# Kernel tuning notes

Measured on AMD Instinct MI355X. Metric: run time of the kernel, lower is better.

The kernel has to match this reference:

```python
import jax, jax.numpy as jnp
import numpy as np

B, T, C, H = 2, 2048, 1024, 16
Dh = C // H  # 64
EPS = 1e-5


def layer_norm(x, g, b):
    mu = jnp.mean(x, axis=-1, keepdims=True)
    var = jnp.mean(jnp.square(x - mu), axis=-1, keepdims=True)
    return (x - mu) * jax.lax.rsqrt(var + EPS) * g + b


def setup_inputs() -> dict:
    key = jax.random.key(0)
    ks = jax.random.split(key, 12)
    s = 0.02
    return {
        "x": jax.random.normal(ks[0], (B, T, C), dtype=jnp.float32),
        # per-head projections, stacked: (H, C, Dh), no bias (bias=False in source)
        "Wq": jax.random.normal(ks[1], (H, C, Dh), dtype=jnp.float32) * s,
        "Wk": jax.random.normal(ks[2], (H, C, Dh), dtype=jnp.float32) * s,
        "Wv": jax.random.normal(ks[3], (H, C, Dh), dtype=jnp.float32) * s,
        "Wo": jax.random.normal(ks[4], (H * Dh, C), dtype=jnp.float32) * s,
        "bo": jnp.zeros((C,), dtype=jnp.float32),
        "W1": jax.random.normal(ks[5], (C, 4 * C), dtype=jnp.float32) * s,
        "b1": jnp.zeros((4 * C,), dtype=jnp.float32),
        "W2": jax.random.normal(ks[6], (4 * C, C), dtype=jnp.float32) * s,
        "b2": jnp.zeros((C,), dtype=jnp.float32),
        "g1": jnp.ones((C,), dtype=jnp.float32),
        "be1": jnp.zeros((C,), dtype=jnp.float32),
        "g2": jnp.ones((C,), dtype=jnp.float32),
        "be2": jnp.zeros((C,), dtype=jnp.float32),
    }


def reference(x, Wq, Wk, Wv, Wo, bo, W1, b1, W2, b2, g1, be1, g2, be2):
    # --- self-attention sublayer ---
    h = layer_norm(x, g1, be1)                       # (B,T,C)
    q = jnp.einsum("btc,hcd->bhtd", h, Wq)
    k = jnp.einsum("btc,hcd->bhtd", h, Wk)
    v = jnp.einsum("btc,hcd->bhtd", h, Wv)
    # NOTE: source scales by C**-0.5 (head INPUT dim), not head_size**-0.5
    scores = jnp.einsum("bhqd,bhkd->bhqk", q, k) * (C ** -0.5)
    # encoder=True default => mask is all ones => no masking applied
    w = jax.nn.softmax(scores, axis=-1)              # (B,H,T,T)
    o = jnp.einsum("bhqk,bhkd->bhqd", w, v)          # (B,H,T,Dh)
    o = o.transpose(0, 2, 1, 3).reshape(B, T, H * Dh)  # concat heads
    attn = o @ Wo + bo                               # output projection
    x = x + attn
    # --- feed-forward sublayer ---
    h2 = layer_norm(x, g2, be2)
    ff = jax.nn.relu(h2 @ W1 + b1) @ W2 + b2
    return x + ff
```

## Files before the change

### kernel.cpp

```cpp
#include <hip/hip_runtime.h>
#include <hip/hip_bf16.h>

#define BT   4096
#define CD   1024
#define TD   2048
#define NH   16
#define DH   64
#define BB   2

typedef __attribute__((ext_vector_type(8))) short bf16x8;
typedef __attribute__((ext_vector_type(4))) short bf16x4;
typedef __attribute__((ext_vector_type(4))) float f32x4;
typedef __attribute__((ext_vector_type(2))) unsigned int u32x2;
typedef __attribute__((ext_vector_type(4))) unsigned int u32x4;

__device__ inline short f2bf(float f) {
    union { float fv; unsigned u; } x; x.fv = f;
    unsigned r = x.u + 0x7fffu + ((x.u >> 16) & 1u);
    return (short)(r >> 16);
}
__device__ inline float bf2f(short s) {
    union { unsigned u; float f; } x; x.u = ((unsigned)(unsigned short)s) << 16;
    return x.f;
}
__device__ inline unsigned pk2bf(float a, float b) {
    union { __hip_bfloat162 h; unsigned u; } cv;
    cv.h = __float22bfloat162_rn(float2{a, b});
    return cv.u;
}

#if __has_builtin(__builtin_amdgcn_exp2f)
#define EXP2(x) __builtin_amdgcn_exp2f(x)
#else
#define EXP2(x) exp2f(x)
#endif

__device__ inline void gload_lds16(const short* g, short* lds) {
    __builtin_amdgcn_global_load_lds(
        (const __attribute__((address_space(1))) void*)g,
        (__attribute__((address_space(3))) void*)lds, 16, 0, 0);
}

__launch_bounds__(256)
__global__ void ln_kernel(const float* __restrict__ x,
                          const float* __restrict__ g,
                          const float* __restrict__ be,
                          short* __restrict__ out) {
    __shared__ float red[2][4];
    const int row = blockIdx.x;
    const int c4 = threadIdx.x * 4;
    const float* xr = x + (size_t)row * CD;
    float4 v = *(const float4*)&xr[c4];
    float s  = (v.x + v.y) + (v.z + v.w);
    float ss = (v.x * v.x + v.y * v.y) + (v.z * v.z + v.w * v.w);
    #pragma unroll
    for (int off = 32; off > 0; off >>= 1) {
        s  += __shfl_down(s,  off, 64);
        ss += __shfl_down(ss, off, 64);
    }
    int wid = threadIdx.x >> 6, lane = threadIdx.x & 63;
    if (lane == 0) { red[0][wid] = s; red[1][wid] = ss; }
    __syncthreads();
    float sum   = red[0][0] + red[0][1] + red[0][2] + red[0][3];
    float sumsq = red[1][0] + red[1][1] + red[1][2] + red[1][3];
    float mu   = sum * (1.f / CD);
    float var  = sumsq * (1.f / CD) - mu * mu;
    float rstd = rsqrtf(var + 1e-5f);
    float4 gv = *(const float4*)&g[c4];
    float4 bv = *(const float4*)&be[c4];
    bf16x4 o;
    o[0] = f2bf((v.x - mu) * rstd * gv.x + bv.x);
    o[1] = f2bf((v.y - mu) * rstd * gv.y + bv.y);
    o[2] = f2bf((v.z - mu) * rstd * gv.z + bv.z);
    o[3] = f2bf((v.w - mu) * rstd * gv.w + bv.w);
    *(bf16x4*)&out[(size_t)row * CD + c4] = o;
}

__launch_bounds__(256)
__global__ void prep_weights(const float* __restrict__ Wq, const float* __restrict__ Wk,
                             const float* __restrict__ Wv, const float* __restrict__ Wo,
                             const float* __restrict__ W1, const float* __restrict__ W2,
                             short* __restrict__ wqt, short* __restrict__ wot,
                             short* __restrict__ w1t, short* __restrict__ w2t) {
    __shared__ float tt[64][65];
    const int id = blockIdx.x;
    const float* in; short* out; int R, Cc, r0, c0;
    if (id < 768) {
        int which = id >> 8, rem = id & 255, hh = rem >> 4, ry = rem & 15;
        in  = (which == 0 ? Wq : which == 1 ? Wk : Wv) + (size_t)hh * CD * DH;
        out = wqt + (size_t)which * CD * CD + (size_t)hh * DH * CD;
        R = CD; Cc = DH; r0 = ry * 64; c0 = 0;
    } else if (id < 1024) {
        int t = id - 768;  in = Wo; out = wot; R = CD;     Cc = CD;     r0 = (t >> 4) * 64; c0 = (t & 15) * 64;
    } else if (id < 2048) {
        int t = id - 1024; in = W1; out = w1t; R = CD;     Cc = 4 * CD; r0 = (t >> 6) * 64; c0 = (t & 63) * 64;
    } else {
        int t = id - 2048; in = W2; out = w2t; R = 4 * CD; Cc = CD;     r0 = (t >> 4) * 64; c0 = (t & 15) * 64;
    }
    const int tid = threadIdx.x;
    #pragma unroll
    for (int i = 0; i < 4; ++i) {
        int f = i * 256 + tid;
        int r = f >> 4, cc = (f & 15) * 4;
        float4 vv = *(const float4*)&in[(size_t)(r0 + r) * Cc + c0 + cc];
        tt[r][cc]     = vv.x;
        tt[r][cc + 1] = vv.y;
        tt[r][cc + 2] = vv.z;
        tt[r][cc + 3] = vv.w;
    }
    __syncthreads();
    #pragma unroll
    for (int i = 0; i < 16; ++i) {
        int e = i * 256 + tid;
        out[(size_t)(c0 + (e >> 6)) * R + r0 + (e & 63)] = f2bf(tt[e & 63][e >> 6]);
    }
}

__launch_bounds__(256)
__global__ void vtrans(const short* __restrict__ vin, short* __restrict__ vout) {
    __shared__ short t[64 * 65];
    const int tid = threadIdx.x;
    const int bh = blockIdx.y;
    const int t0 = blockIdx.x * 64;
    const int b = bh >> 4, h = bh & 15;
    const short* src = vin + (size_t)b * TD * CD + (size_t)h * DH;
    short* dst = vout + (size_t)bh * DH * TD;
    #pragma unroll
    for (int i = 0; i < 16; ++i) {
        int e = i * 256 + tid;
        t[(e >> 6) * 65 + (e & 63)] = src[(size_t)(t0 + (e >> 6)) * CD + (e & 63)];
    }
    __syncthreads();
    #pragma unroll
    for (int i = 0; i < 16; ++i) {
        int e = i * 256 + tid;
        int d = e >> 6, tt = e & 63;
        dst[(size_t)d * TD + t0 + tt] = t[tt * 65 + d];
    }
}

template <int MODE, int TN, int GR>
__launch_bounds__(GR * 256)
__global__ void gemm_mfma(const short* __restrict__ A,
                          const short* __restrict__ Bt,
                          const float* __restrict__ bias,
                          const float* __restrict__ resid,
                          float* __restrict__ outf,
                          short* __restrict__ outb,
                          int N, int K) {
    constexpr int NBUF = (GR == 2) ? 4 : 3;
    __shared__ __align__(16) short smem[GR * NBUF * (128 + TN) * 32];
    const int tid = threadIdx.x;
    const int kgrp = (GR == 2) ? (tid >> 8) : 0;
    const int tid256 = tid & 255;
    const int w4 = tid256 >> 6, lane = tid & 63;
    const int quad = lane >> 4, l16 = lane & 15;
    const int wr = w4 >> 1, wc = w4 & 1;
    const int li = blockIdx.y * gridDim.x + blockIdx.x;
    const int m0 = ((li & 7) * 4 + ((li >> 3) & 3)) * 128;
    const int n0 = (li >> 5) * TN;
    const int NT = TN / 32;
    const int kbase = kgrp * (K / GR);

    short* grpBase = smem + (size_t)kgrp * NBUF * (128 + TN) * 32;
#define AS(bi) (grpBase + (bi) * (128 + TN) * 32)
#define BS(bi) (AS(bi) + 128 * 32)

    f32x4 acc[4][NT] = {};

    auto STAGE = [&](int kt, int bi) {
        const int k0 = kbase + kt * 32;
        short* as = AS(bi);
        short* bs = BS(bi);
        #pragma unroll
        for (int i = 0; i < 2; ++i) {
            int s = i * 256 + tid256;
            int row = s >> 2, kc = (s & 3) ^ ((row >> 1) & 3);
            gload_lds16(A + (size_t)(m0 + row) * K + k0 + kc * 8,
                        &as[(i * 256 + w4 * 64) * 8]);
        }
        #pragma unroll
        for (int i = 0; i < TN / 64; ++i) {
            int s = i * 256 + tid256;
            int row = s >> 2, kc = (s & 3) ^ ((row >> 1) & 3);
            gload_lds16(Bt + (size_t)(n0 + row) * K + k0 + kc * 8,
                        &bs[(i * 256 + w4 * 64) * 8]);
        }
    };

    auto COMPUTE = [&](int bi) {
        const int xo = (quad ^ ((l16 >> 1) & 3)) * 8;
        const short* as = AS(bi);
        const short* bs = BS(bi);
        bf16x8 a[4], b[NT];
        #pragma unroll
        for (int mt = 0; mt < 4; ++mt)
            a[mt] = *(const bf16x8*)&as[(wr * 64 + mt * 16 + l16) * 32 + xo];
        #pragma unroll
        for (int nt = 0; nt < NT; ++nt)
            b[nt] = *(const bf16x8*)&bs[(wc * (TN / 2) + nt * 16 + l16) * 32 + xo];
        #pragma unroll
        for (int mt = 0; mt < 4; ++mt)
            #pragma unroll
            for (int nt = 0; nt < NT; ++nt)
                acc[mt][nt] = __builtin_amdgcn_mfma_f32_16x16x32_bf16(a[mt], b[nt], acc[mt][nt], 0, 0, 0);
    };

    const int nk = (K / GR) >> 5;
    if (GR == 2) {
        STAGE(0, 0);
        STAGE(1, 1);
        STAGE(2, 2);
        for (int t = 0; t < nk - 2; ++t) {
            asm volatile("s_waitcnt vmcnt(8)" ::: "memory");
            __builtin_amdgcn_s_barrier();
            asm volatile("" ::: "memory");
            if (t + 3 < nk) STAGE(t + 3, (t + 3) & 3);
            COMPUTE(t & 3);
        }
        asm volatile("s_waitcnt vmcnt(4)" ::: "memory");
        __builtin_amdgcn_s_barrier();
        asm volatile("" ::: "memory");
        COMPUTE((nk - 2) & 3);
        asm volatile("s_waitcnt vmcnt(0)" ::: "memory");
        __builtin_amdgcn_s_barrier();
        asm volatile("" ::: "memory");
        COMPUTE((nk - 1) & 3);
    } else {
        STAGE(0, 0);
        STAGE(1, 1);
        int bi = 0;
        for (int t = 0; t < nk - 1; ++t) {
            if (TN == 256) asm volatile("s_waitcnt vmcnt(6)" ::: "memory");
            else           asm volatile("s_waitcnt vmcnt(4)" ::: "memory");
            __builtin_amdgcn_s_barrier();
            asm volatile("" ::: "memory");
            int bn = bi + 2 >= 3 ? bi - 1 : bi + 2;
            if (t + 2 < nk) STAGE(t + 2, bn);
            COMPUTE(bi);
            bi = bi + 1 >= 3 ? 0 : bi + 1;
        }
        asm volatile("s_waitcnt vmcnt(0)" ::: "memory");
        __builtin_amdgcn_s_barrier();
        asm volatile("" ::: "memory");
        COMPUTE(bi);
    }

    if (GR == 2) {
        float* red = (float*)smem;
        __syncthreads();
        if (kgrp == 1) {
            #pragma unroll
            for (int mt = 0; mt < 4; ++mt)
                #pragma unroll
                for (int nt = 0; nt < NT; ++nt)
                    *(f32x4*)&red[((mt * NT + nt) * 256 + w4 * 64 + lane) * 4] = acc[mt][nt];
        }
        __syncthreads();
        if (kgrp == 1) return;
        #pragma unroll
        for (int mt = 0; mt < 4; ++mt)
            #pragma unroll
            for (int nt = 0; nt < NT; ++nt) {
                f32x4 p = *(const f32x4*)&red[((mt * NT + nt) * 256 + w4 * 64 + lane) * 4];
                acc[mt][nt] += p;
            }
    }

    const float qsc = (MODE == 5 && n0 < CD) ? 0.03125f * 1.44269504f : 1.0f;
    short* ob5 = (MODE == 5) ? outb + (size_t)(n0 >> 10) * BT * CD : nullptr;

    #pragma unroll
    for (int mt = 0; mt < 4; ++mt)
        #pragma unroll
        for (int nt = 0; nt < NT; ++nt)
            #pragma unroll
            for (int reg = 0; reg < 4; ++reg) {
                int row = m0 + wr * 64 + mt * 16 + quad * 4 + reg;
                int col = n0 + wc * (TN / 2) + nt * 16 + l16;
                float v = acc[mt][nt][reg];
                if (MODE == 1) { v += bias[col] + resid[(size_t)row * N + col];
                                 outf[(size_t)row * N + col] = v; }
                if (MODE == 2) { v = fmaxf(v + bias[col], 0.f);
                                 outb[(size_t)row * N + col] = f2bf(v); }
                if (MODE == 5) { ob5[(size_t)row * CD + (col & 1023)] = f2bf(v * qsc); }
            }
#undef AS
#undef BS
}

#define BQ   128
#define BK   32

__launch_bounds__(256, 5)
__global__ void attn_mfma(const short* __restrict__ q,
                          const short* __restrict__ k,
                          const short* __restrict__ vt,
                          short* __restrict__ opart,
                          float* __restrict__ lpart) {
    __shared__ short Ks[4][BK * DH];
    __shared__ short Vt[4][DH * BK];

    const int tid  = threadIdx.x;
    const int w = tid >> 6, lane = tid & 63;
    const int quad = lane >> 4, l16 = lane & 15;
    const int h = blockIdx.y;
    const int b = blockIdx.z >> 1, split = blockIdx.z & 1;
    const int q0 = blockIdx.x * BQ;
    const size_t base  = (size_t)b * TD * CD + (size_t)h * DH;
    const size_t vbase = (size_t)(b * NH + h) * DH * TD;

    bf16x8 qf[2][2];
    #pragma unroll
    for (int rt = 0; rt < 2; ++rt) {
        const short* qp = q + base + (size_t)(q0 + w * 32 + rt * 16 + l16) * CD;
        qf[rt][0] = *(const bf16x8*)&qp[quad * 8];
        qf[rt][1] = *(const bf16x8*)&qp[32 + quad * 8];
    }

    const bf16x8 ones = {(short)0x3F80, (short)0x3F80, (short)0x3F80, (short)0x3F80,
                         (short)0x3F80, (short)0x3F80, (short)0x3F80, (short)0x3F80};
    f32x4 O_l[2] = {};
    f32x4 O[2][4] = {};

    const int kbeg = split * (TD / 2);
    const int NTI = (TD / 2) / BK;

    const int ks  = tid >> 3;
    const int kc  = (tid & 7) ^ (ks & 7);
    const int kkey = (((ks & 15) >> 2) << 3) + (ks & 3) + ((ks >> 4) << 2);
    const short* kgp = k + base + (size_t)kkey * CD + kc * 8;
    const int vd = tid >> 2;
    const int vc = (tid & 3) ^ ((vd >> 1) & 3);
    const short* vgp = vt + vbase + (size_t)vd * TD + vc * 8;

#define STAGE_T(kt, bi) do {                                              \
        const size_t ko_ = (size_t)(kbeg + (kt) * BK);                    \
        gload_lds16(kgp + ko_ * CD, &Ks[bi][w * 512]);                    \
        gload_lds16(vgp + ko_,      &Vt[bi][w * 512]);                    \
    } while (0)

#define COMPUTE_T(bi) do {                                                \
        __builtin_amdgcn_s_setprio(1);                                    \
        const int kswz = l16 & 7;                                         \
        bf16x8 kbe0 = *(const bf16x8*)&Ks[bi][l16 * 64 + ((quad) ^ kswz) * 8];        \
        bf16x8 kbe1 = *(const bf16x8*)&Ks[bi][l16 * 64 + ((4 + quad) ^ kswz) * 8];    \
        bf16x8 kbo0 = *(const bf16x8*)&Ks[bi][(16 + l16) * 64 + ((quad) ^ kswz) * 8]; \
        bf16x8 kbo1 = *(const bf16x8*)&Ks[bi][(16 + l16) * 64 + ((4 + quad) ^ kswz) * 8]; \
        bf16x8 pa8[2];                                                    \
        _Pragma("unroll")                                                 \
        for (int rt = 0; rt < 2; ++rt) {                                  \
            f32x4 ae = (f32x4){0.f, 0.f, 0.f, 0.f};                       \
            f32x4 ao = (f32x4){0.f, 0.f, 0.f, 0.f};                       \
            ae = __builtin_amdgcn_mfma_f32_16x16x32_bf16(kbe0, qf[rt][0], ae, 0, 0, 0); \
            ae = __builtin_amdgcn_mfma_f32_16x16x32_bf16(kbe1, qf[rt][1], ae, 0, 0, 0); \
            ao = __builtin_amdgcn_mfma_f32_16x16x32_bf16(kbo0, qf[rt][0], ao, 0, 0, 0); \
            ao = __builtin_amdgcn_mfma_f32_16x16x32_bf16(kbo1, qf[rt][1], ao, 0, 0, 0); \
            float pe0 = EXP2(ae[0]), pe1 = EXP2(ae[1]);                   \
            float pe2 = EXP2(ae[2]), pe3 = EXP2(ae[3]);                   \
            float po0 = EXP2(ao[0]), po1 = EXP2(ao[1]);                   \
            float po2 = EXP2(ao[2]), po3 = EXP2(ao[3]);                   \
            union { u32x4 u; bf16x8 s; } cv_;                             \
            cv_.u = (u32x4){pk2bf(pe0, pe1), pk2bf(pe2, pe3),             \
                            pk2bf(po0, po1), pk2bf(po2, po3)};            \
            pa8[rt] = cv_.s;                                              \
        }                                                                 \
        const int vswz = (l16 >> 1) & 3;                                  \
        _Pragma("unroll")                                                 \
        for (int dt = 0; dt < 4; ++dt) {                                  \
            bf16x8 vb = *(const bf16x8*)&Vt[bi][(dt * 16 + l16) * 32 + ((quad) ^ vswz) * 8]; \
            O[0][dt] = __builtin_amdgcn_mfma_f32_16x16x32_bf16(pa8[0], vb, O[0][dt], 0, 0, 0); \
            O[1][dt] = __builtin_amdgcn_mfma_f32_16x16x32_bf16(pa8[1], vb, O[1][dt], 0, 0, 0); \
        }                                                                 \
        O_l[0] = __builtin_amdgcn_mfma_f32_16x16x32_bf16(pa8[0], ones, O_l[0], 0, 0, 0); \
        O_l[1] = __builtin_amdgcn_mfma_f32_16x16x32_bf16(pa8[1], ones, O_l[1], 0, 0, 0); \
        __builtin_amdgcn_s_setprio(0);                                    \
    } while (0)

    STAGE_T(0, 0);
    STAGE_T(1, 1);
    STAGE_T(2, 2);
    for (int t = 0; t < NTI - 2; ++t) {
        asm volatile("s_waitcnt vmcnt(4)" ::: "memory");
        __builtin_amdgcn_s_barrier();
        asm volatile("" ::: "memory");
        if (t + 3 < NTI) STAGE_T(t + 3, (t + 3) & 3);
        COMPUTE_T(t & 3);
    }
    asm volatile("s_waitcnt vmcnt(2)" ::: "memory");
    __builtin_amdgcn_s_barrier();
    asm volatile("" ::: "memory");
    COMPUTE_T((NTI - 2) & 3);
    asm volatile("s_waitcnt vmcnt(0)" ::: "memory");
    __builtin_amdgcn_s_barrier();
    asm volatile("" ::: "memory");
    COMPUTE_T((NTI - 1) & 3);
#undef STAGE_T
#undef COMPUTE_T

    short* osp = opart + (size_t)split * BT * CD;
    float* lsp = lpart + (size_t)split * BB * NH * TD + (size_t)(b * NH + h) * TD;
    #pragma unroll
    for (int rt = 0; rt < 2; ++rt) {
        if (l16 == 0)
            *(f32x4*)&lsp[q0 + w * 32 + rt * 16 + quad * 4] = O_l[rt];
        #pragma unroll
        for (int reg = 0; reg < 4; ++reg) {
            int row = q0 + w * 32 + rt * 16 + quad * 4 + reg;
            short* op = osp + base + (size_t)row * CD;
            #pragma unroll
            for (int dt = 0; dt < 4; ++dt)
                op[dt * 16 + l16] = f2bf(O[rt][dt][reg]);
        }
    }
}

__launch_bounds__(256)
__global__ void attn_combine(const short* __restrict__ opart,
                             const float* __restrict__ lpart,
                             short* __restrict__ ob) {
    const size_t idx = ((size_t)blockIdx.x * 256 + threadIdx.x) * 8;
    const int row = (int)(idx >> 10);
    const int col = (int)(idx & 1023);
    const int b = row >> 11, qq = row & (TD - 1), hh = col >> 6;
    const size_t lbase = (size_t)(b * NH + hh) * TD + qq;
    const float l0 = lpart[lbase];
    const float l1 = lpart[(size_t)BB * NH * TD + lbase];
    const float inv = 1.f / (l0 + l1);
    bf16x8 a = *(const bf16x8*)&opart[idx];
    bf16x8 c = *(const bf16x8*)&opart[(size_t)BT * CD + idx];
    bf16x8 r;
    #pragma unroll
    for (int j = 0; j < 8; ++j)
        r[j] = f2bf((bf2f(a[j]) + bf2f(c[j])) * inv);
    *(bf16x8*)&ob[idx] = r;
}

extern "C" void kernel_launch(void* const* d_in, const int* in_sizes, int n_in,
                              void* d_out, int out_size, void* d_ws, size_t ws_size,
                              hipStream_t stream) {
    const float* x   = (const float*)d_in[0];
    const float* Wq  = (const float*)d_in[1];
    const float* Wk  = (const float*)d_in[2];
    const float* Wv  = (const float*)d_in[3];
    const float* Wo  = (const float*)d_in[4];
    const float* bo  = (const float*)d_in[5];
    const float* W1  = (const float*)d_in[6];
    const float* b1  = (const float*)d_in[7];
    const float* W2  = (const float*)d_in[8];
    const float* b2  = (const float*)d_in[9];
    const float* g1  = (const float*)d_in[10];
    const float* be1 = (const float*)d_in[11];
    const float* g2  = (const float*)d_in[12];
    const float* be2 = (const float*)d_in[13];
    float* out = (float*)d_out;

    const size_t SZ = (size_t)BT * CD;
    float* ws  = (float*)d_ws;
    short* qbf = (short*)ws;
    short* kbf = qbf + SZ;
    short* vbf = qbf + 2 * SZ;
    float* lpart = ws + SZ + SZ / 2;
    short* opart = (short*)(ws + 2 * SZ);
    float* x1  = ws + 2 * SZ;
    short* h   = (short*)(ws + 3 * SZ);
    short* ob  = (short*)(ws + 3 * SZ + SZ / 2);
    short* wqt = (short*)(ws + 4 * SZ);
    short* wot = wqt + 3 * CD * CD;
    short* w1t = (short*)(ws + 4 * SZ + SZ / 2);
    short* w2t = (short*)(ws + 5 * SZ);
    short* vtg = (short*)(ws + 5 * SZ + SZ / 2);
    short* ff1 = (short*)ws;

    ln_kernel<<<BT, 256, 0, stream>>>(x, g1, be1, h);

    prep_weights<<<3072, 256, 0, stream>>>(Wq, Wk, Wv, Wo, W1, W2, wqt, wot, w1t, w2t);

    gemm_mfma<5, 128, 1><<<dim3(24, 32), 256, 0, stream>>>(h, wqt, nullptr, nullptr, nullptr, qbf, 3 * CD, CD);

    vtrans<<<dim3(TD / 64, 2 * NH), 256, 0, stream>>>(vbf, vtg);

    attn_mfma<<<dim3(TD / BQ, NH, BB * 2), 256, 0, stream>>>(qbf, kbf, vtg, opart, lpart);

    attn_combine<<<dim3((int)(SZ / (256 * 8))), 256, 0, stream>>>(opart, lpart, ob);

    gemm_mfma<1, 128, 2><<<dim3(8, 32), 512, 0, stream>>>(ob, wot, bo, x, x1, nullptr, CD, CD);

    ln_kernel<<<BT, 256, 0, stream>>>(x1, g2, be2, h);

    gemm_mfma<2, 256, 1><<<dim3(16, 32), 256, 0, stream>>>(h, w1t, b1, nullptr, nullptr, ff1, 4 * CD, CD);

    gemm_mfma<1, 128, 2><<<dim3(8, 32), 512, 0, stream>>>(ff1, w2t, b2, x1, out, nullptr, CD, 4 * CD);
}
```

Baseline: 322.5 us.

## Split W2 GEMM K across four wave groups and shrink attention pipeline depth

Adds a GR=4 intra-block split-K variant of the MFMA GEMM. It uses 1024 threads, double buffering, and a staged shared-memory reduction across the four K groups, and applies it to the FFN down-projection (K=4096). The attention kernel drops from four to three K/V LDS buffers with a rotating prefetch of depth two, which cuts LDS use per block and may allow more resident blocks. In exchange, the split-K path adds barriers and reduction traffic, and the shallower prefetch in attention can expose more memory latency.

```diff
diff --git a/kernel.cpp b/kernel.cpp
--- a/kernel.cpp
+++ b/kernel.cpp
@@ -148,10 +148,10 @@
                           float* __restrict__ outf,
                           short* __restrict__ outb,
                           int N, int K) {
-    constexpr int NBUF = (GR == 2) ? 4 : 3;
+    constexpr int NBUF = (GR == 2) ? 4 : ((GR == 4) ? 2 : 3);
     __shared__ __align__(16) short smem[GR * NBUF * (128 + TN) * 32];
     const int tid = threadIdx.x;
-    const int kgrp = (GR == 2) ? (tid >> 8) : 0;
+    const int kgrp = (GR > 1) ? (tid >> 8) : 0;
     const int tid256 = tid & 255;
     const int w4 = tid256 >> 6, lane = tid & 63;
     const int quad = lane >> 4, l16 = lane & 15;
@@ -207,7 +207,23 @@
     };
 
     const int nk = (K / GR) >> 5;
-    if (GR == 2) {
+    if (GR == 4) {
+        STAGE(0, 0);
+        STAGE(1, 1);
+        for (int t = 0; t < nk - 1; ++t) {
+            asm volatile("s_waitcnt vmcnt(4)" ::: "memory");
+            __builtin_amdgcn_s_barrier();
+            asm volatile("" ::: "memory");
+            COMPUTE(t & 1);
+            __builtin_amdgcn_s_barrier();
+            asm volatile("" ::: "memory");
+            if (t + 2 < nk) STAGE(t + 2, t & 1);
+        }
+        asm volatile("s_waitcnt vmcnt(0)" ::: "memory");
+        __builtin_amdgcn_s_barrier();
+        asm volatile("" ::: "memory");
+        COMPUTE((nk - 1) & 1);
+    } else if (GR == 2) {
         STAGE(0, 0);
         STAGE(1, 1);
         STAGE(2, 2);
@@ -246,7 +262,30 @@
         COMPUTE(bi);
     }
 
-    if (GR == 2) {
+    if (GR == 4) {
+        float* red = (float*)smem;
+        #pragma unroll
+        for (int mt = 0; mt < 4; ++mt) {
+            __syncthreads();
+            if (kgrp != 0) {
+                #pragma unroll
+                for (int nt = 0; nt < NT; ++nt)
+                    *(f32x4*)&red[(size_t)(kgrp - 1) * 4096 + (nt * 256 + w4 * 64 + lane) * 4] = acc[mt][nt];
+            }
+            __syncthreads();
+            if (kgrp == 0) {
+                #pragma unroll
+                for (int nt = 0; nt < NT; ++nt) {
+                    int off = (nt * 256 + w4 * 64 + lane) * 4;
+                    f32x4 p1 = *(const f32x4*)&red[off];
+                    f32x4 p2 = *(const f32x4*)&red[4096 + off];
+                    f32x4 p3 = *(const f32x4*)&red[8192 + off];
+                    acc[mt][nt] += (p1 + p2) + p3;
+                }
+            }
+        }
+        if (kgrp != 0) return;
+    } else if (GR == 2) {
         float* red = (float*)smem;
         __syncthreads();
         if (kgrp == 1) {
@@ -298,8 +337,8 @@
                           const short* __restrict__ vt,
                           short* __restrict__ opart,
                           float* __restrict__ lpart) {
-    __shared__ short Ks[4][BK * DH];
-    __shared__ short Vt[4][DH * BK];
+    __shared__ short Ks[3][BK * DH];
+    __shared__ short Vt[3][DH * BK];
 
     const int tid  = threadIdx.x;
     const int w = tid >> 6, lane = tid & 63;
@@ -379,22 +418,20 @@
 
     STAGE_T(0, 0);
     STAGE_T(1, 1);
-    STAGE_T(2, 2);
-    for (int t = 0; t < NTI - 2; ++t) {
-        asm volatile("s_waitcnt vmcnt(4)" ::: "memory");
+    int bi = 0;
+    for (int t = 0; t < NTI - 1; ++t) {
+        asm volatile("s_waitcnt vmcnt(2)" ::: "memory");
         __builtin_amdgcn_s_barrier();
         asm volatile("" ::: "memory");
-        if (t + 3 < NTI) STAGE_T(t + 3, (t + 3) & 3);
-        COMPUTE_T(t & 3);
-    }
-    asm volatile("s_waitcnt vmcnt(2)" ::: "memory");
-    __builtin_amdgcn_s_barrier();
-    asm volatile("" ::: "memory");
-    COMPUTE_T((NTI - 2) & 3);
+        int bn = bi + 2 >= 3 ? bi - 1 : bi + 2;
+        if (t + 2 < NTI) STAGE_T(t + 2, bn);
+        COMPUTE_T(bi);
+        bi = bi + 1 >= 3 ? 0 : bi + 1;
+    }
     asm volatile("s_waitcnt vmcnt(0)" ::: "memory");
     __builtin_amdgcn_s_barrier();
     asm volatile("" ::: "memory");
-    COMPUTE_T((NTI - 1) & 3);
+    COMPUTE_T(bi);
 #undef STAGE_T
 #undef COMPUTE_T
 
@@ -490,5 +527,5 @@
 
     gemm_mfma<2, 256, 1><<<dim3(16, 32), 256, 0, stream>>>(h, w1t, b1, nullptr, nullptr, ff1, 4 * CD, CD);
 
-    gemm_mfma<1, 128, 2><<<dim3(8, 32), 512, 0, stream>>>(ff1, w2t, b2, x1, out, nullptr, CD, 4 * CD);
-}
+    gemm_mfma<1, 128, 4><<<dim3(8, 32), 1024, 0, stream>>>(ff1, w2t, b2, x1, out, nullptr, CD, 4 * CD);
+}
```

Result: no change. 328.1 us (+1.7%).

## Add 256x256-tile GEMM for FFN up-projection and triple-buffer attention pipeline

Applied to the files above, without the earlier changes.

Adds a new 512-thread GEMM kernel with 256x256 output tiles, 3-stage LDS buffering and a swizzled block-to-tile mapping, and uses it for the W1 up-projection with bias and ReLU. Larger tiles raise arithmetic intensity and cut redundant global loads of A and B. The attention kernel also moves from a 4-deep to a 3-deep K/V ring buffer with prefetch distance 2, which lowers LDS use and may raise occupancy but hides less latency. The new GEMM launches only 256 blocks at one block per CU, so occupancy is low.

```diff
diff --git a/kernel.cpp b/kernel.cpp
--- a/kernel.cpp
+++ b/kernel.cpp
@@ -289,6 +289,97 @@
 #undef BS
 }
 
+__launch_bounds__(512, 1)
+__global__ void gemm_256(const short* __restrict__ A,
+                         const short* __restrict__ Bt,
+                         const float* __restrict__ bias,
+                         short* __restrict__ outb,
+                         int N, int K) {
+    __shared__ __align__(16) short smem[3 * 512 * 32];
+    const int tid = threadIdx.x;
+    const int w = tid >> 6, lane = tid & 63;
+    const int quad = lane >> 4, l16 = lane & 15;
+    const int wr = w >> 2, wc = w & 3;
+    const int li = blockIdx.x;
+    const int m0 = ((li & 7) * 2 + ((li >> 3) & 1)) * 256;
+    const int n0 = (li >> 4) * 256;
+
+#define AS6(bi) (smem + (bi) * 512 * 32)
+#define BS6(bi) (AS6(bi) + 256 * 32)
+
+    f32x4 acc[8][4] = {};
+
+    auto STAGE = [&](int kt, int bi) {
+        const int k0 = kt * 32;
+        short* as = AS6(bi);
+        short* bs = BS6(bi);
+        #pragma unroll
+        for (int i = 0; i < 2; ++i) {
+            int s = i * 512 + tid;
+            int row = s >> 2, kc = (s & 3) ^ ((row >> 1) & 3);
+            gload_lds16(A + (size_t)(m0 + row) * K + k0 + kc * 8,
+                        &as[(i * 512 + w * 64) * 8]);
+        }
+        #pragma unroll
+        for (int i = 0; i < 2; ++i) {
+            int s = i * 512 + tid;
+            int row = s >> 2, kc = (s & 3) ^ ((row >> 1) & 3);
+            gload_lds16(Bt + (size_t)(n0 + row) * K + k0 + kc * 8,
+                        &bs[(i * 512 + w * 64) * 8]);
+        }
+    };
+
+    auto COMPUTE = [&](int bi) {
+        const int xo = (quad ^ ((l16 >> 1) & 3)) * 8;
+        const short* as = AS6(bi);
+        const short* bs = BS6(bi);
+        bf16x8 a[8], b[4];
+        #pragma unroll
+        for (int mt = 0; mt < 8; ++mt)
+            a[mt] = *(const bf16x8*)&as[(wr * 128 + mt * 16 + l16) * 32 + xo];
+        #pragma unroll
+        for (int nt = 0; nt < 4; ++nt)
+            b[nt] = *(const bf16x8*)&bs[(wc * 64 + nt * 16 + l16) * 32 + xo];
+        #pragma unroll
+        for (int mt = 0; mt < 8; ++mt)
+            #pragma unroll
+            for (int nt = 0; nt < 4; ++nt)
+                acc[mt][nt] = __builtin_amdgcn_mfma_f32_16x16x32_bf16(a[mt], b[nt], acc[mt][nt], 0, 0, 0);
+    };
+
+    const int nk = K >> 5;
+    STAGE(0, 0);
+    STAGE(1, 1);
+    int bi = 0;
+    for (int t = 0; t < nk - 1; ++t) {
+        asm volatile("s_waitcnt vmcnt(4)" ::: "memory");
+        __builtin_amdgcn_s_barrier();
+        asm volatile("" ::: "memory");
+        int bn = bi + 2 >= 3 ? bi - 1 : bi + 2;
+        if (t + 2 < nk) STAGE(t + 2, bn);
+        COMPUTE(bi);
+        bi = bi + 1 >= 3 ? 0 : bi + 1;
+    }
+    asm volatile("s_waitcnt vmcnt(0)" ::: "memory");
+    __builtin_amdgcn_s_barrier();
+    asm volatile("" ::: "memory");
+    COMPUTE(bi);
+
+    #pragma unroll
+    for (int mt = 0; mt < 8; ++mt)
+        #pragma unroll
+        for (int nt = 0; nt < 4; ++nt)
+            #pragma unroll
+            for (int reg = 0; reg < 4; ++reg) {
+                int row = m0 + wr * 128 + mt * 16 + quad * 4 + reg;
+                int col = n0 + wc * 64 + nt * 16 + l16;
+                float v = fmaxf(acc[mt][nt][reg] + bias[col], 0.f);
+                outb[(size_t)row * N + col] = f2bf(v);
+            }
+#undef AS6
+#undef BS6
+}
+
 #define BQ   128
 #define BK   32
 
@@ -298,8 +389,8 @@
                           const short* __restrict__ vt,
                           short* __restrict__ opart,
                           float* __restrict__ lpart) {
-    __shared__ short Ks[4][BK * DH];
-    __shared__ short Vt[4][DH * BK];
+    __shared__ short Ks[3][BK * DH];
+    __shared__ short Vt[3][DH * BK];
 
     const int tid  = threadIdx.x;
     const int w = tid >> 6, lane = tid & 63;
@@ -379,22 +470,20 @@
 
     STAGE_T(0, 0);
     STAGE_T(1, 1);
-    STAGE_T(2, 2);
-    for (int t = 0; t < NTI - 2; ++t) {
-        asm volatile("s_waitcnt vmcnt(4)" ::: "memory");
+    int bi = 0;
+    for (int t = 0; t < NTI - 1; ++t) {
+        asm volatile("s_waitcnt vmcnt(2)" ::: "memory");
         __builtin_amdgcn_s_barrier();
         asm volatile("" ::: "memory");
-        if (t + 3 < NTI) STAGE_T(t + 3, (t + 3) & 3);
-        COMPUTE_T(t & 3);
-    }
-    asm volatile("s_waitcnt vmcnt(2)" ::: "memory");
-    __builtin_amdgcn_s_barrier();
-    asm volatile("" ::: "memory");
-    COMPUTE_T((NTI - 2) & 3);
+        int bn = bi + 2 >= 3 ? bi - 1 : bi + 2;
+        if (t + 2 < NTI) STAGE_T(t + 2, bn);
+        COMPUTE_T(bi);
+        bi = bi + 1 >= 3 ? 0 : bi + 1;
+    }
     asm volatile("s_waitcnt vmcnt(0)" ::: "memory");
     __builtin_amdgcn_s_barrier();
     asm volatile("" ::: "memory");
-    COMPUTE_T((NTI - 1) & 3);
+    COMPUTE_T(bi);
 #undef STAGE_T
 #undef COMPUTE_T
 
@@ -488,7 +577,7 @@
 
     ln_kernel<<<BT, 256, 0, stream>>>(x1, g2, be2, h);
 
-    gemm_mfma<2, 256, 1><<<dim3(16, 32), 256, 0, stream>>>(h, w1t, b1, nullptr, nullptr, ff1, 4 * CD, CD);
+    gemm_256<<<256, 512, 0, stream>>>(h, w1t, b1, ff1, 4 * CD, CD);
 
     gemm_mfma<1, 128, 2><<<dim3(8, 32), 512, 0, stream>>>(ff1, w2t, b2, x1, out, nullptr, CD, 4 * CD);
 }
```

After: 313.5 us. -2.8%, faster.
